# Optimization experiments

Measured on AMD Instinct MI355X. Metric: run time of the kernel, lower is better.

## Reference

```python
import jax, jax.numpy as jnp
import numpy as np

K, B, L, D_IN, H = 4, 16, 4096, 512, 128

def setup_inputs() -> dict:
    key = jax.random.key(0)
    k1, k2, k3, k4, k5 = jax.random.split(key, 5)
    hs = jax.random.normal(k1, (K, B, L, D_IN), dtype=jnp.float32)
    mask = jax.random.randint(k2, (B, L), 0, 2, dtype=jnp.int32)
    # xavier-ish scaled params
    ln_w = jax.random.normal(k3, (H, D_IN + H), dtype=jnp.float32) * (1.0 / np.sqrt(D_IN + H))
    ln_b = jnp.zeros((H,), dtype=jnp.float32)
    v_w = jax.random.normal(k4, (H,), dtype=jnp.float32) * (1.0 / np.sqrt(H))
    vq = jax.random.normal(k5, (H,), dtype=jnp.float32) * (1.0 / np.sqrt(H))
    return {"hs": hs, "mask": mask, "ln_w": ln_w, "ln_b": ln_b, "v_w": v_w, "vq": vq}

def reference(hs, mask, ln_w, ln_b, v_w, vq):
    # hs: [K,B,L,D], mask: [B,L], ln_w: [H, D+H], vq/v_w/ln_b: [H]
    d = hs.shape[-1]
    W_h = ln_w[:, :d]        # [H, D]
    W_q = ln_w[:, d:]        # [H, H]
    # Linear over concat([hs, vq]) == hs @ W_h.T + W_q @ vq + b (vq is constant per position)
    q_bias = W_q @ vq + ln_b                      # [H]
    h = jnp.tanh(jnp.einsum('kbld,hd->kblh', hs, W_h) + q_bias)
    s = jnp.einsum('kblh,h->kbl', h, v_w)         # [K,B,L]
    s = s - (mask[None] == 0).astype(s.dtype) * 10000.0
    a = jax.nn.softmax(s, axis=0)                 # softmax over the K (stack) axis
    x = jnp.einsum('kbl,kbld->bld', a, hs)        # weighted sum over K
    return x  # dropout is identity in eval mode
```

## Files before the change

kernel.cpp:

```cpp
#include <hip/hip_runtime.h>
#include <hip/hip_bf16.h>
#include <stdint.h>

#define KK 4
#define BB 16
#define LL 4096
#define DD 512
#define HH 128

typedef __attribute__((ext_vector_type(8))) short bf16x8;
typedef __attribute__((ext_vector_type(4))) float f32x4;
typedef __attribute__((ext_vector_type(4))) unsigned int u32x4;

__device__ __forceinline__ unsigned int pack_bf16(float lo, float hi) {
  unsigned int a = __float_as_uint(lo);
  unsigned int b = __float_as_uint(hi);
  a = (a + 0x7FFFu + ((a >> 16) & 1u)) >> 16;
  b = (b + 0x7FFFu + ((b >> 16) & 1u)) >> 16;
  return a | (b << 16);
}

__device__ __forceinline__ void bar_lds() {
  __builtin_amdgcn_sched_barrier(0);
  asm volatile("s_waitcnt lgkmcnt(0)" ::: "memory");
  __builtin_amdgcn_s_barrier();
  __builtin_amdgcn_sched_barrier(0);
}

template <int N>
__device__ __forceinline__ float dpp_shr_add(float x) {
  int y = __builtin_amdgcn_update_dpp(0, __float_as_int(x), 0x110 | N, 0xF, 0xF,
                                      true);
  return x + __int_as_float(y);
}

__global__ void qbias_kernel(const float* __restrict__ ln_w,
                             const float* __restrict__ ln_b,
                             const float* __restrict__ vq,
                             float* __restrict__ qb) {
  int h = threadIdx.x;
  if (h < HH) {
    float acc = ln_b[h];
    const float* wq = ln_w + (size_t)h * (DD + HH) + DD;
    for (int j = 0; j < HH; ++j) acc = fmaf(wq[j], vq[j], acc);
    qb[h] = acc;
  }
}

__global__ void wf_kernel(const float* __restrict__ ln_w,
                          unsigned int* __restrict__ wf) {
  int gid = blockIdx.x * 256 + threadIdx.x;
  int ks = gid >> 9;
  int nt = (gid >> 6) & 7;
  int lane = gid & 63;
  int h = nt * 16 + (lane & 15);
  int d0 = ks * 32 + (lane >> 4) * 8;
  const float* src = ln_w + (size_t)h * (DD + HH) + d0;
  u32x4 v;
  v.x = pack_bf16(src[0], src[1]);
  v.y = pack_bf16(src[2], src[3]);
  v.z = pack_bf16(src[4], src[5]);
  v.w = pack_bf16(src[6], src[7]);
  *(u32x4*)(wf + (size_t)gid * 4) = v;
}

__global__ __launch_bounds__(256, 2) void agg_main(
    const float* __restrict__ hs, const unsigned int* __restrict__ wf,
    const float* __restrict__ qb, const float* __restrict__ vw,
    float* __restrict__ out) {
  extern __shared__ char smem[];
  char* buf0 = smem;
  char* buf1 = smem + 16384;
  f32x4* spv = (f32x4*)(smem + 32768);

  const int tid = threadIdx.x;
  const int lane = tid & 63;
  const int wv = tid >> 6;
  const int r = lane & 15;
  const int cg = lane >> 4;
  const int ntA = wv * 2, ntB = ntA + 1;

  const int b = blockIdx.x >> 5;
  const int l0b = (blockIdx.x & 31) << 7;

  bf16x8 wregA[16], wregB[16];
#pragma unroll
  for (int ks = 0; ks < 16; ++ks) {
    wregA[ks] = *(const bf16x8*)(wf + ((size_t)((ks * 8 + ntA) * 64 + lane)) * 4);
    wregB[ks] = *(const bf16x8*)(wf + ((size_t)((ks * 8 + ntB) * 64 + lane)) * 4);
  }

  const float qbrA = qb[ntA * 16 + r], qbrB = qb[ntB * 16 + r];
  const float vwrA = vw[ntA * 16 + r], vwrB = vw[ntB * 16 + r];

  f32x4 sv[8];
  auto issue_stage = [&](int l0) {
#pragma unroll
    for (int i = 0; i < 4; ++i) {
      int row = i * 4 + wv;
      int k = row & 3, pos = row >> 2;
      int d0 = (lane ^ (row & 7)) * 8;
      const float* p = hs + (((size_t)(k * BB + b)) * LL + l0 + pos) * DD + d0;
      sv[i * 2]     = *(const f32x4*)(p);
      sv[i * 2 + 1] = *(const f32x4*)(p + 4);
    }
  };
  auto write_stage = [&](char* dst) {
#pragma unroll
    for (int i = 0; i < 4; ++i) {
      u32x4 pk;
      pk.x = pack_bf16(sv[i * 2].x, sv[i * 2].y);
      pk.y = pack_bf16(sv[i * 2].z, sv[i * 2].w);
      pk.z = pack_bf16(sv[i * 2 + 1].x, sv[i * 2 + 1].y);
      pk.w = pack_bf16(sv[i * 2 + 1].z, sv[i * 2 + 1].w);
      *(u32x4*)(dst + i * 4096 + tid * 16) = pk;
    }
  };

  issue_stage(l0b);
  write_stage(buf0);
  bar_lds();

  for (int t = 0; t < 32; ++t) {
    const int l0 = l0b + t * 4;
    char* cur = (t & 1) ? buf1 : buf0;
    char* nxt = (t & 1) ? buf0 : buf1;

    if (t < 31) issue_stage(l0 + 4);

    f32x4 accA = {0.f, 0.f, 0.f, 0.f};
    f32x4 accB = {0.f, 0.f, 0.f, 0.f};
    const int swz = (r & 7) << 4;
#pragma unroll
    for (int ks = 0; ks < 16; ++ks) {
      bf16x8 a = *(const bf16x8*)(cur + r * 1024 + ((ks * 64 + cg * 16) ^ swz));
      accA = __builtin_amdgcn_mfma_f32_16x16x32_bf16(a, wregA[ks], accA, 0, 0, 0);
      accB = __builtin_amdgcn_mfma_f32_16x16x32_bf16(a, wregB[ks], accB, 0, 0, 0);
    }

    float ps[4];
#pragma unroll
    for (int j = 0; j < 4; ++j) {
      float zA = accA[j] + qbrA;
      zA = fminf(15.f, fmaxf(-15.f, zA));
      float eA = __expf(-2.f * zA);
      float thA = (1.f - eA) * __builtin_amdgcn_rcpf(1.f + eA);
      float zB = accB[j] + qbrB;
      zB = fminf(15.f, fmaxf(-15.f, zB));
      float eB = __expf(-2.f * zB);
      float thB = (1.f - eB) * __builtin_amdgcn_rcpf(1.f + eB);
      ps[j] = fmaf(vwrA, thA, vwrB * thB);
    }
#pragma unroll
    for (int j = 0; j < 4; ++j) {
      ps[j] = dpp_shr_add<1>(ps[j]);
      ps[j] = dpp_shr_add<2>(ps[j]);
      ps[j] = dpp_shr_add<4>(ps[j]);
      ps[j] = dpp_shr_add<8>(ps[j]);
    }
    if (r == 15) {
      f32x4 v = {ps[0], ps[1], ps[2], ps[3]};
      spv[cg * 4 + wv] = v;
    }
    bar_lds();

    float a0, a1, a2, a3;
    {
      f32x4 s = spv[wv * 4 + 0];
      s += spv[wv * 4 + 1];
      s += spv[wv * 4 + 2];
      s += spv[wv * 4 + 3];
      float mx = fmaxf(fmaxf(s.x, s.y), fmaxf(s.z, s.w));
      float e0 = __expf(s.x - mx), e1 = __expf(s.y - mx);
      float e2 = __expf(s.z - mx), e3 = __expf(s.w - mx);
      float inv = __builtin_amdgcn_rcpf(e0 + e1 + e2 + e3);
      a0 = e0 * inv; a1 = e1 * inv; a2 = e2 * inv; a3 = e3 * inv;
    }

    {
      float x[8];
#pragma unroll
      for (int j = 0; j < 8; ++j) x[j] = 0.f;
#pragma unroll
      for (int k = 0; k < 4; ++k) {
        int row = wv * 4 + k;
        float ak = k == 0 ? a0 : (k == 1 ? a1 : (k == 2 ? a2 : a3));
        u32x4 u = *(const u32x4*)(cur + row * 1024 +
                                  ((lane * 16) ^ ((row & 7) << 4)));
        x[0] = fmaf(ak, __uint_as_float(u.x << 16), x[0]);
        x[1] = fmaf(ak, __uint_as_float(u.x & 0xffff0000u), x[1]);
        x[2] = fmaf(ak, __uint_as_float(u.y << 16), x[2]);
        x[3] = fmaf(ak, __uint_as_float(u.y & 0xffff0000u), x[3]);
        x[4] = fmaf(ak, __uint_as_float(u.z << 16), x[4]);
        x[5] = fmaf(ak, __uint_as_float(u.z & 0xffff0000u), x[5]);
        x[6] = fmaf(ak, __uint_as_float(u.w << 16), x[6]);
        x[7] = fmaf(ak, __uint_as_float(u.w & 0xffff0000u), x[7]);
      }
      float* ob = out + (((size_t)b) * LL + l0 + wv) * DD + lane * 8;
      f32x4 o0 = {x[0], x[1], x[2], x[3]};
      f32x4 o1 = {x[4], x[5], x[6], x[7]};
      __builtin_nontemporal_store(o0, (f32x4*)ob);
      __builtin_nontemporal_store(o1, (f32x4*)(ob + 4));
    }

    if (t < 31) write_stage(nxt);
    bar_lds();
  }
}

extern "C" void kernel_launch(void* const* d_in, const int* in_sizes, int n_in,
                              void* d_out, int out_size, void* d_ws, size_t ws_size,
                              hipStream_t stream) {
  const float* hs   = (const float*)d_in[0];
  const float* ln_w = (const float*)d_in[2];
  const float* ln_b = (const float*)d_in[3];
  const float* v_w  = (const float*)d_in[4];
  const float* vq   = (const float*)d_in[5];
  float* out = (float*)d_out;

  unsigned int* wf = (unsigned int*)d_ws;
  float* qb = (float*)((char*)d_ws + 131072);

  qbias_kernel<<<1, 128, 0, stream>>>(ln_w, ln_b, vq, qb);
  wf_kernel<<<32, 256, 0, stream>>>(ln_w, wf);
  agg_main<<<512, 256, 33024, stream>>>(hs, wf, qb, v_w, out);
}
```

Baseline: 150.0 us.

## Stream hs directly into LDS as fp32 via global_load_lds with larger blocks

Replaces the register-staged load, bf16 pack and LDS write with asynchronous global_load_lds DMA of fp32 rows straight into double-buffered LDS. Blocks grow to 512 threads covering 8 positions per step, and the bf16 conversion moves into the MFMA operand read. The weighted sum now reads fp32 from LDS, which also changes numerics toward the reference. The cost is 128KB of LDS per block, which limits occupancy to one block per CU, and a full vmcnt wait at each step that may expose load latency.

```diff
diff --git a/kernel.cpp b/kernel.cpp
--- a/kernel.cpp
+++ b/kernel.cpp
@@ -27,11 +27,24 @@
   __builtin_amdgcn_sched_barrier(0);
 }
 
+__device__ __forceinline__ void bar_full() {
+  __builtin_amdgcn_sched_barrier(0);
+  asm volatile("s_waitcnt vmcnt(0) lgkmcnt(0)" ::: "memory");
+  __builtin_amdgcn_s_barrier();
+  __builtin_amdgcn_sched_barrier(0);
+}
+
 template <int N>
 __device__ __forceinline__ float dpp_shr_add(float x) {
   int y = __builtin_amdgcn_update_dpp(0, __float_as_int(x), 0x110 | N, 0xF, 0xF,
                                       true);
   return x + __int_as_float(y);
+}
+
+__device__ __forceinline__ void load_lds16(const void* g, void* l) {
+  __builtin_amdgcn_global_load_lds(
+      (const __attribute__((address_space(1))) unsigned int*)g,
+      (__attribute__((address_space(3))) unsigned int*)l, 16, 0, 0);
 }
 
 __global__ void qbias_kernel(const float* __restrict__ ln_w,
@@ -64,24 +77,26 @@
   *(u32x4*)(wf + (size_t)gid * 4) = v;
 }
 
-__global__ __launch_bounds__(256, 2) void agg_main(
+__global__ __launch_bounds__(512) void agg_main(
     const float* __restrict__ hs, const unsigned int* __restrict__ wf,
     const float* __restrict__ qb, const float* __restrict__ vw,
     float* __restrict__ out) {
   extern __shared__ char smem[];
   char* buf0 = smem;
-  char* buf1 = smem + 16384;
-  f32x4* spv = (f32x4*)(smem + 32768);
+  char* buf1 = smem + 65536;
+  f32x4* spv = (f32x4*)(smem + 131072);
 
   const int tid = threadIdx.x;
   const int lane = tid & 63;
   const int wv = tid >> 6;
   const int r = lane & 15;
   const int cg = lane >> 4;
-  const int ntA = wv * 2, ntB = ntA + 1;
-
-  const int b = blockIdx.x >> 5;
-  const int l0b = (blockIdx.x & 31) << 7;
+  const int st = wv & 1;
+  const int pr = wv >> 1;
+  const int ntA = pr * 2, ntB = ntA + 1;
+
+  const int b = blockIdx.x >> 4;
+  const int l0b = (blockIdx.x & 15) << 8;
 
   bf16x8 wregA[16], wregB[16];
 #pragma unroll
@@ -93,49 +108,48 @@
   const float qbrA = qb[ntA * 16 + r], qbrB = qb[ntB * 16 + r];
   const float vwrA = vw[ntA * 16 + r], vwrB = vw[ntB * 16 + r];
 
-  f32x4 sv[8];
-  auto issue_stage = [&](int l0) {
-#pragma unroll
-    for (int i = 0; i < 4; ++i) {
-      int row = i * 4 + wv;
+  auto issue_stage = [&](int l0, char* dst) {
+#pragma unroll
+    for (int i = 0; i < 8; ++i) {
+      int chunk = wv * 8 + i;
+      int row = chunk >> 1;
+      int half = chunk & 1;
       int k = row & 3, pos = row >> 2;
-      int d0 = (lane ^ (row & 7)) * 8;
-      const float* p = hs + (((size_t)(k * BB + b)) * LL + l0 + pos) * DD + d0;
-      sv[i * 2]     = *(const f32x4*)(p);
-      sv[i * 2 + 1] = *(const f32x4*)(p + 4);
-    }
+      int gbyte = (half * 1024 + lane * 16) ^ ((row & 7) << 5);
+      const char* p = (const char*)(hs +
+          (((size_t)(k * BB + b)) * LL + l0 + pos) * DD) + gbyte;
+      load_lds16(p, dst + chunk * 1024);
+    }
+    __builtin_amdgcn_sched_barrier(0);
   };
-  auto write_stage = [&](char* dst) {
-#pragma unroll
-    for (int i = 0; i < 4; ++i) {
-      u32x4 pk;
-      pk.x = pack_bf16(sv[i * 2].x, sv[i * 2].y);
-      pk.y = pack_bf16(sv[i * 2].z, sv[i * 2].w);
-      pk.z = pack_bf16(sv[i * 2 + 1].x, sv[i * 2 + 1].y);
-      pk.w = pack_bf16(sv[i * 2 + 1].z, sv[i * 2 + 1].w);
-      *(u32x4*)(dst + i * 4096 + tid * 16) = pk;
-    }
-  };
-
-  issue_stage(l0b);
-  write_stage(buf0);
-  bar_lds();
+
+  issue_stage(l0b, buf0);
+  bar_full();
 
   for (int t = 0; t < 32; ++t) {
-    const int l0 = l0b + t * 4;
+    const int l0 = l0b + t * 8;
     char* cur = (t & 1) ? buf1 : buf0;
     char* nxt = (t & 1) ? buf0 : buf1;
 
-    if (t < 31) issue_stage(l0 + 4);
+    if (t < 31) issue_stage(l0 + 8, nxt);
 
     f32x4 accA = {0.f, 0.f, 0.f, 0.f};
     f32x4 accB = {0.f, 0.f, 0.f, 0.f};
-    const int swz = (r & 7) << 4;
+    const int abase = (st * 16 + r) * 2048;
+    const int swz = (r & 7) << 5;
 #pragma unroll
     for (int ks = 0; ks < 16; ++ks) {
-      bf16x8 a = *(const bf16x8*)(cur + r * 1024 + ((ks * 64 + cg * 16) ^ swz));
-      accA = __builtin_amdgcn_mfma_f32_16x16x32_bf16(a, wregA[ks], accA, 0, 0, 0);
-      accB = __builtin_amdgcn_mfma_f32_16x16x32_bf16(a, wregB[ks], accB, 0, 0, 0);
+      int off = (ks * 128 + cg * 32) ^ swz;
+      f32x4 a0 = *(const f32x4*)(cur + abase + off);
+      f32x4 a1 = *(const f32x4*)(cur + abase + off + 16);
+      u32x4 pk;
+      pk.x = pack_bf16(a0.x, a0.y);
+      pk.y = pack_bf16(a0.z, a0.w);
+      pk.z = pack_bf16(a1.x, a1.y);
+      pk.w = pack_bf16(a1.z, a1.w);
+      bf16x8 af = __builtin_bit_cast(bf16x8, pk);
+      accA = __builtin_amdgcn_mfma_f32_16x16x32_bf16(af, wregA[ks], accA, 0, 0, 0);
+      accB = __builtin_amdgcn_mfma_f32_16x16x32_bf16(af, wregB[ks], accB, 0, 0, 0);
     }
 
     float ps[4];
@@ -160,7 +174,7 @@
     }
     if (r == 15) {
       f32x4 v = {ps[0], ps[1], ps[2], ps[3]};
-      spv[cg * 4 + wv] = v;
+      spv[(st * 4 + cg) * 4 + pr] = v;
     }
     bar_lds();
 
@@ -185,16 +199,17 @@
       for (int k = 0; k < 4; ++k) {
         int row = wv * 4 + k;
         float ak = k == 0 ? a0 : (k == 1 ? a1 : (k == 2 ? a2 : a3));
-        u32x4 u = *(const u32x4*)(cur + row * 1024 +
-                                  ((lane * 16) ^ ((row & 7) << 4)));
-        x[0] = fmaf(ak, __uint_as_float(u.x << 16), x[0]);
-        x[1] = fmaf(ak, __uint_as_float(u.x & 0xffff0000u), x[1]);
-        x[2] = fmaf(ak, __uint_as_float(u.y << 16), x[2]);
-        x[3] = fmaf(ak, __uint_as_float(u.y & 0xffff0000u), x[3]);
-        x[4] = fmaf(ak, __uint_as_float(u.z << 16), x[4]);
-        x[5] = fmaf(ak, __uint_as_float(u.z & 0xffff0000u), x[5]);
-        x[6] = fmaf(ak, __uint_as_float(u.w << 16), x[6]);
-        x[7] = fmaf(ak, __uint_as_float(u.w & 0xffff0000u), x[7]);
+        int off = (lane * 32) ^ ((row & 7) << 5);
+        f32x4 v0 = *(const f32x4*)(cur + row * 2048 + off);
+        f32x4 v1 = *(const f32x4*)(cur + row * 2048 + off + 16);
+        x[0] = fmaf(ak, v0.x, x[0]);
+        x[1] = fmaf(ak, v0.y, x[1]);
+        x[2] = fmaf(ak, v0.z, x[2]);
+        x[3] = fmaf(ak, v0.w, x[3]);
+        x[4] = fmaf(ak, v1.x, x[4]);
+        x[5] = fmaf(ak, v1.y, x[5]);
+        x[6] = fmaf(ak, v1.z, x[6]);
+        x[7] = fmaf(ak, v1.w, x[7]);
       }
       float* ob = out + (((size_t)b) * LL + l0 + wv) * DD + lane * 8;
       f32x4 o0 = {x[0], x[1], x[2], x[3]};
@@ -203,8 +218,7 @@
       __builtin_nontemporal_store(o1, (f32x4*)(ob + 4));
     }
 
-    if (t < 31) write_stage(nxt);
-    bar_lds();
+    bar_full();
   }
 }
 
@@ -223,5 +237,5 @@
 
   qbias_kernel<<<1, 128, 0, stream>>>(ln_w, ln_b, vq, qb);
   wf_kernel<<<32, 256, 0, stream>>>(ln_w, wf);
-  agg_main<<<512, 256, 33024, stream>>>(hs, wf, qb, v_w, out);
-}
+  agg_main<<<256, 512, 131584, stream>>>(hs, wf, qb, v_w, out);
+}
```

New measurement: 151.2 us. Within noise of the previous version (+0.8%).
